# Kernel optimization log

Hardware: AMD Instinct MI355X
Metric: run time of the kernel (lower is better)

The kernel has to match this reference:

```python
import jax, jax.numpy as jnp
import numpy as np

AGENT_TYPE_VEHICLE = 1
AGENT_TYPE_PEDESTRIAN = 2
N_VEHICLE_INTENTIONS = 6
N_PEDESTRIAN_INTENTIONS = 2
INTENTION_LOGIT_DIM = 6


def setup_inputs() -> dict:
    key = jax.random.key(0)
    ks = jax.random.split(key, 10)
    B, N, D = 32, 2048, 512
    H = D // 2
    s_in = 1.0 / np.sqrt(D)
    s_h = 1.0 / np.sqrt(H)
    return {
        "repr3": jax.random.normal(ks[0], (B, N, D), dtype=jnp.float32),
        "agent_type_ids": jax.random.randint(ks[1], (B, N), 0, 4, dtype=jnp.int64),
        # vehicle head: Linear(D, D//2) -> GELU -> Linear(D//2, 6)
        "vW1": jax.random.normal(ks[2], (H, D), dtype=jnp.float32) * s_in,
        "vb1": jax.random.normal(ks[3], (H,), dtype=jnp.float32) * s_in,
        "vW2": jax.random.normal(ks[4], (N_VEHICLE_INTENTIONS, H), dtype=jnp.float32) * s_h,
        "vb2": jax.random.normal(ks[5], (N_VEHICLE_INTENTIONS,), dtype=jnp.float32) * s_h,
        # pedestrian head: Linear(D, D//2) -> GELU -> Linear(D//2, 2)
        "pW1": jax.random.normal(ks[6], (H, D), dtype=jnp.float32) * s_in,
        "pb1": jax.random.normal(ks[7], (H,), dtype=jnp.float32) * s_in,
        "pW2": jax.random.normal(ks[8], (N_PEDESTRIAN_INTENTIONS, H), dtype=jnp.float32) * s_h,
        "pb2": jax.random.normal(ks[9], (N_PEDESTRIAN_INTENTIONS,), dtype=jnp.float32) * s_h,
    }


def _mlp(x, W1, b1, W2, b2):
    # x: [B,N,D] -> [B,N,out]; exact (erf) GELU matches torch nn.GELU()
    h = jax.nn.gelu(jnp.einsum("bnd,hd->bnh", x, W1) + b1, approximate=False)
    return jnp.einsum("bnh,oh->bno", h, W2) + b2


def reference(repr3, agent_type_ids, vW1, vb1, vW2, vb2, pW1, pb1, pW2, pb2):
    v_mask = agent_type_ids == AGENT_TYPE_VEHICLE  # [B,N]
    p_mask = agent_type_ids == AGENT_TYPE_PEDESTRIAN
    v_logits = _mlp(repr3, vW1, vb1, vW2, vb2)  # [B,N,6]
    p_logits = _mlp(repr3, pW1, pb1, pW2, pb2)  # [B,N,2]
    pad = INTENTION_LOGIT_DIM - N_PEDESTRIAN_INTENTIONS
    p_padded = jnp.pad(p_logits, ((0, 0), (0, 0), (0, pad)))  # [B,N,6]
    zero = jnp.zeros((), dtype=repr3.dtype)
    intention_logits = (
        jnp.where(v_mask[..., None], v_logits, zero)
        + jnp.where(p_mask[..., None], p_padded, zero)
    )
    return intention_logits, v_mask, p_mask
```

## Files before the change

### kernel.cpp

```cpp
#include <hip/hip_runtime.h>
#include <hip/hip_bf16.h>
#include <math.h>


#define TOKENS 65536
#define DIM    512
#define HID    256
#define BK     32
#define ASTR   40
#define HSTR   264

using short8 = __attribute__((ext_vector_type(8))) short;
using f32x4  = __attribute__((ext_vector_type(4))) float;

__device__ __forceinline__ unsigned int pkrne(float a, float b) {
    unsigned int ua = __float_as_uint(a);
    unsigned int ub = __float_as_uint(b);
    ua += 0x7FFFu + ((ua >> 16) & 1u);
    ub += 0x7FFFu + ((ub >> 16) & 1u);
    return (ub & 0xFFFF0000u) | (ua >> 16);
}

__device__ __forceinline__ uint2 cvt4(f32x4 v) {
    return make_uint2(pkrne(v[0], v[1]), pkrne(v[2], v[3]));
}

__device__ __forceinline__ short8 cvt8(const float* __restrict__ p) {
    f32x4 a = *(const f32x4*)p;
    f32x4 b = *(const f32x4*)(p + 4);
    union { unsigned int u[4]; short8 s; } r;
    r.u[0] = pkrne(a[0], a[1]);
    r.u[1] = pkrne(a[2], a[3]);
    r.u[2] = pkrne(b[0], b[1]);
    r.u[3] = pkrne(b[2], b[3]);
    return r.s;
}

__device__ __forceinline__ float gelu_exact(float x) {
    return 0.5f * x * (1.0f + erff(x * 0.7071067811865475f));
}

__global__ __launch_bounds__(256, 2)
void intention_heads_kernel(const float* __restrict__ X,
                            const int* __restrict__ ids,
                            const float* __restrict__ vW1,
                            const float* __restrict__ vb1,
                            const float* __restrict__ vW2,
                            const float* __restrict__ vb2,
                            const float* __restrict__ pW1,
                            const float* __restrict__ pb1,
                            const float* __restrict__ pW2,
                            const float* __restrict__ pb2,
                            float* __restrict__ out)
{
    __shared__ __align__(16) unsigned char smem[64 * HSTR * 2];
    __hip_bfloat16* At = (__hip_bfloat16*)smem;
    __hip_bfloat16* Bt = (__hip_bfloat16*)(smem + 64 * ASTR * 2);
    __hip_bfloat16* H  = (__hip_bfloat16*)smem;

    const int bx   = blockIdx.x;
    const int head = bx & 1;
    const int row0 = (bx >> 1) * 64;

    const int tid  = threadIdx.x;
    const int wave = tid >> 6;
    const int lane = tid & 63;
    const int quad = lane >> 4;
    const int l16  = lane & 15;
    const int wcol = wave * 64;

    const float* W1 = head ? pW1 : vW1;
    const float* b1 = head ? pb1 : vb1;

    const int q   = tid & 7;
    const int r0t = tid >> 3;
    const float* Xs  = X  + (long)(row0 + r0t) * DIM + q * 4;
    const float* W1s = W1 + (long)r0t * DIM + q * 4;

    f32x4 pa[2], pb[8];
    #define LOADTILE(k0)                                              \
        do {                                                          \
            pa[0] = *(const f32x4*)(Xs + (k0));                       \
            pa[1] = *(const f32x4*)(Xs + 32 * DIM + (k0));            \
            _Pragma("unroll")                                         \
            for (int e = 0; e < 8; ++e)                               \
                pb[e] = *(const f32x4*)(W1s + e * 32 * DIM + (k0));   \
        } while (0)

    f32x4 acc[4][4];
    #pragma unroll
    for (int i = 0; i < 4; ++i)
        #pragma unroll
        for (int j = 0; j < 4; ++j)
            acc[i][j] = (f32x4){0.f, 0.f, 0.f, 0.f};

    LOADTILE(0);

    for (int it = 0; it < DIM / BK; ++it) {
        *(uint2*)&At[(r0t)      * ASTR + q * 4] = cvt4(pa[0]);
        *(uint2*)&At[(r0t + 32) * ASTR + q * 4] = cvt4(pa[1]);
        #pragma unroll
        for (int e = 0; e < 8; ++e)
            *(uint2*)&Bt[(r0t + 32 * e) * ASTR + q * 4] = cvt4(pb[e]);
        __syncthreads();

        short8 af[4], bf_[4];
        #pragma unroll
        for (int i = 0; i < 4; ++i)
            af[i] = *(const short8*)&At[(i * 16 + l16) * ASTR + quad * 8];
        #pragma unroll
        for (int j = 0; j < 4; ++j)
            bf_[j] = *(const short8*)&Bt[(wcol + j * 16 + l16) * ASTR + quad * 8];

        if (it + 1 < DIM / BK)
            LOADTILE((it + 1) * BK);

        #pragma unroll
        for (int i = 0; i < 4; ++i)
            #pragma unroll
            for (int j = 0; j < 4; ++j)
                acc[i][j] = __builtin_amdgcn_mfma_f32_16x16x32_bf16(af[i], bf_[j], acc[i][j], 0, 0, 0);
        __syncthreads();
    }

    float b1v[4];
    #pragma unroll
    for (int j = 0; j < 4; ++j)
        b1v[j] = b1[wcol + j * 16 + l16];

    #pragma unroll
    for (int i = 0; i < 4; ++i) {
        #pragma unroll
        for (int j = 0; j < 4; ++j) {
            const int col = wcol + j * 16 + l16;
            #pragma unroll
            for (int r = 0; r < 4; ++r) {
                const int row = i * 16 + quad * 4 + r;
                float v = acc[i][j][r] + b1v[j];
                union { unsigned int u; struct { short lo, hi; } s; } t;
                t.u = pkrne(v == v ? gelu_exact(v) : 0.f, 0.f);
                H[row * HSTR + col] = *(__hip_bfloat16*)&t.s.lo;
            }
        }
    }
    __syncthreads();

    const float* W2 = head ? pW2 : vW2;
    const float* b2 = head ? pb2 : vb2;
    const int nOut = head ? 2 : 6;

    f32x4 acc2 = (f32x4){0.f, 0.f, 0.f, 0.f};
    const int tokb = wave * 16;
    const short* hbase = (const short*)&H[(tokb + l16) * HSTR + quad * 8];
    #pragma unroll
    for (int k0 = 0; k0 < HID; k0 += 32) {
        short8 af = *(const short8*)(hbase + k0);
        short8 bfrag = (short8){0, 0, 0, 0, 0, 0, 0, 0};
        if (l16 < nOut)
            bfrag = cvt8(W2 + l16 * HID + k0 + quad * 8);
        acc2 = __builtin_amdgcn_mfma_f32_16x16x32_bf16(af, bfrag, acc2, 0, 0, 0);
    }

    const float b2v = (l16 < nOut) ? b2[l16] : 0.0f;

    #pragma unroll
    for (int r = 0; r < 4; ++r) {
        const int t = row0 + tokb + quad * 4 + r;
        const int type = ids[t];
        if (head == 0) {
            if (l16 == 0) {
                out[TOKENS * 6 + t] = (type == 1) ? 1.0f : 0.0f;
                out[TOKENS * 7 + t] = (type == 2) ? 1.0f : 0.0f;
            }
            if (l16 < 6) {
                if (type == 1)
                    out[t * 6 + l16] = acc2[r] + b2v;
                else if (type != 2)
                    out[t * 6 + l16] = 0.0f;
            }
        } else {
            if (l16 < 6 && type == 2)
                out[t * 6 + l16] = (l16 < 2) ? (acc2[r] + b2v) : 0.0f;
        }
    }
}

extern "C" void kernel_launch(void* const* d_in, const int* in_sizes, int n_in,
                              void* d_out, int out_size, void* d_ws, size_t ws_size,
                              hipStream_t stream) {
    (void)n_in; (void)out_size; (void)d_ws; (void)ws_size;
    const float* X   = (const float*)d_in[0];
    const int*   ids = (const int*)d_in[1];
    const float* vW1 = (const float*)d_in[2];
    const float* vb1 = (const float*)d_in[3];
    const float* vW2 = (const float*)d_in[4];
    const float* vb2 = (const float*)d_in[5];
    const float* pW1 = (const float*)d_in[6];
    const float* pb1 = (const float*)d_in[7];
    const float* pW2 = (const float*)d_in[8];
    const float* pb2 = (const float*)d_in[9];
    float* out = (float*)d_out;

    const int tokens = in_sizes[1];
    const int grid   = (tokens / 64) * 2;

    hipLaunchKernelGGL(intention_heads_kernel, dim3(grid), dim3(256), 0, stream,
                       X, ids, vW1, vb1, vW2, vb2, pW1, pb1, pW2, pb2, out);
}
```

Before: 284.4 us.

## Fuse vehicle and pedestrian heads into one 512-thread block sharing X tile

Each block now computes both heads for its 64 tokens: eight waves cover a combined 512-wide hidden layer made of vW1 and pW1, and X is staged into LDS once instead of once per head. The second-layer waves are split between the vehicle and pedestrian outputs. The register prefetch of the next k-tile is dropped, and launch bounds change to (512,4), which may force register spills given the 64-float accumulators. The LDS footprint grows through the wider H buffer. The bf16 packing now uses a perm builtin, and the NaN guard before GELU is removed.

New measurement: 349.8 us. 1.23x slower.

```diff
diff --git a/kernel.cpp b/kernel.cpp
--- a/kernel.cpp
+++ b/kernel.cpp
@@ -6,9 +6,8 @@
 #define TOKENS 65536
 #define DIM    512
 #define HID    256
-#define BK     32
 #define ASTR   40
-#define HSTR   264
+#define HSTR   520
 
 using short8 = __attribute__((ext_vector_type(8))) short;
 using f32x4  = __attribute__((ext_vector_type(4))) float;
@@ -18,7 +17,7 @@
     unsigned int ub = __float_as_uint(b);
     ua += 0x7FFFu + ((ua >> 16) & 1u);
     ub += 0x7FFFu + ((ub >> 16) & 1u);
-    return (ub & 0xFFFF0000u) | (ua >> 16);
+    return __builtin_amdgcn_perm(ub, ua, 0x07060302u);
 }
 
 __device__ __forceinline__ uint2 cvt4(f32x4 v) {
@@ -28,19 +27,24 @@
 __device__ __forceinline__ short8 cvt8(const float* __restrict__ p) {
     f32x4 a = *(const f32x4*)p;
     f32x4 b = *(const f32x4*)(p + 4);
-    union { unsigned int u[4]; short8 s; } r;
-    r.u[0] = pkrne(a[0], a[1]);
-    r.u[1] = pkrne(a[2], a[3]);
-    r.u[2] = pkrne(b[0], b[1]);
-    r.u[3] = pkrne(b[2], b[3]);
+    union { uint2 u[2]; short8 s; } r;
+    r.u[0] = cvt4(a);
+    r.u[1] = cvt4(b);
     return r.s;
+}
+
+__device__ __forceinline__ __hip_bfloat16 bf16rne(float x) {
+    unsigned int u = __float_as_uint(x);
+    u += 0x7FFFu + ((u >> 16) & 1u);
+    unsigned short hs = (unsigned short)(u >> 16);
+    return *(__hip_bfloat16*)&hs;
 }
 
 __device__ __forceinline__ float gelu_exact(float x) {
     return 0.5f * x * (1.0f + erff(x * 0.7071067811865475f));
 }
 
-__global__ __launch_bounds__(256, 2)
+__global__ __launch_bounds__(512, 4)
 void intention_heads_kernel(const float* __restrict__ X,
                             const int* __restrict__ ids,
                             const float* __restrict__ vW1,
@@ -58,9 +62,7 @@
     __hip_bfloat16* Bt = (__hip_bfloat16*)(smem + 64 * ASTR * 2);
     __hip_bfloat16* H  = (__hip_bfloat16*)smem;
 
-    const int bx   = blockIdx.x;
-    const int head = bx & 1;
-    const int row0 = (bx >> 1) * 64;
+    const int row0 = blockIdx.x * 64;
 
     const int tid  = threadIdx.x;
     const int wave = tid >> 6;
@@ -69,23 +71,11 @@
     const int l16  = lane & 15;
     const int wcol = wave * 64;
 
-    const float* W1 = head ? pW1 : vW1;
-    const float* b1 = head ? pb1 : vb1;
-
-    const int q   = tid & 7;
-    const int r0t = tid >> 3;
-    const float* Xs  = X  + (long)(row0 + r0t) * DIM + q * 4;
-    const float* W1s = W1 + (long)r0t * DIM + q * 4;
-
-    f32x4 pa[2], pb[8];
-    #define LOADTILE(k0)                                              \
-        do {                                                          \
-            pa[0] = *(const f32x4*)(Xs + (k0));                       \
-            pa[1] = *(const f32x4*)(Xs + 32 * DIM + (k0));            \
-            _Pragma("unroll")                                         \
-            for (int e = 0; e < 8; ++e)                               \
-                pb[e] = *(const f32x4*)(W1s + e * 32 * DIM + (k0));   \
-        } while (0)
+    const int q = tid & 7;
+    const int r = tid >> 3;
+    const float* Xs = X   + (long)(row0 + r) * DIM + q * 4;
+    const float* Wv = vW1 + (long)r * DIM + q * 4;
+    const float* Wp = pW1 + (long)r * DIM + q * 4;
 
     f32x4 acc[4][4];
     #pragma unroll
@@ -94,14 +84,21 @@
         for (int j = 0; j < 4; ++j)
             acc[i][j] = (f32x4){0.f, 0.f, 0.f, 0.f};
 
-    LOADTILE(0);
-
-    for (int it = 0; it < DIM / BK; ++it) {
-        *(uint2*)&At[(r0t)      * ASTR + q * 4] = cvt4(pa[0]);
-        *(uint2*)&At[(r0t + 32) * ASTR + q * 4] = cvt4(pa[1]);
-        #pragma unroll
-        for (int e = 0; e < 8; ++e)
-            *(uint2*)&Bt[(r0t + 32 * e) * ASTR + q * 4] = cvt4(pb[e]);
+    for (int k0 = 0; k0 < DIM; k0 += 32) {
+        {
+            f32x4 v = *(const f32x4*)(Xs + k0);
+            *(uint2*)&At[r * ASTR + q * 4] = cvt4(v);
+        }
+        #pragma unroll
+        for (int e = 0; e < 4; ++e) {
+            f32x4 v = *(const f32x4*)(Wv + (long)e * 64 * DIM + k0);
+            *(uint2*)&Bt[(r + 64 * e) * ASTR + q * 4] = cvt4(v);
+        }
+        #pragma unroll
+        for (int e = 0; e < 4; ++e) {
+            f32x4 v = *(const f32x4*)(Wp + (long)e * 64 * DIM + k0);
+            *(uint2*)&Bt[(256 + r + 64 * e) * ASTR + q * 4] = cvt4(v);
+        }
         __syncthreads();
 
         short8 af[4], bf_[4];
@@ -111,9 +108,6 @@
         #pragma unroll
         for (int j = 0; j < 4; ++j)
             bf_[j] = *(const short8*)&Bt[(wcol + j * 16 + l16) * ASTR + quad * 8];
-
-        if (it + 1 < DIM / BK)
-            LOADTILE((it + 1) * BK);
 
         #pragma unroll
         for (int i = 0; i < 4; ++i)
@@ -123,10 +117,12 @@
         __syncthreads();
     }
 
+    const float* b1 = (wave < 4) ? vb1 : pb1;
+    const int    bo = (wave < 4) ? wcol : (wcol - 256);
     float b1v[4];
     #pragma unroll
     for (int j = 0; j < 4; ++j)
-        b1v[j] = b1[wcol + j * 16 + l16];
+        b1v[j] = b1[bo + j * 16 + l16];
 
     #pragma unroll
     for (int i = 0; i < 4; ++i) {
@@ -134,24 +130,24 @@
         for (int j = 0; j < 4; ++j) {
             const int col = wcol + j * 16 + l16;
             #pragma unroll
-            for (int r = 0; r < 4; ++r) {
-                const int row = i * 16 + quad * 4 + r;
-                float v = acc[i][j][r] + b1v[j];
-                union { unsigned int u; struct { short lo, hi; } s; } t;
-                t.u = pkrne(v == v ? gelu_exact(v) : 0.f, 0.f);
-                H[row * HSTR + col] = *(__hip_bfloat16*)&t.s.lo;
+            for (int rr = 0; rr < 4; ++rr) {
+                const int row = i * 16 + quad * 4 + rr;
+                H[row * HSTR + col] = bf16rne(gelu_exact(acc[i][j][rr] + b1v[j]));
             }
         }
     }
     __syncthreads();
 
-    const float* W2 = head ? pW2 : vW2;
-    const float* b2 = head ? pb2 : vb2;
-    const int nOut = head ? 2 : 6;
+    const int g     = wave >> 1;
+    const int isPed = wave & 1;
+    const int tokb  = g * 16;
+    const float* W2 = isPed ? pW2 : vW2;
+    const float* b2 = isPed ? pb2 : vb2;
+    const int  nOut = isPed ? 2 : 6;
+    const int  hoff = isPed ? 256 : 0;
 
     f32x4 acc2 = (f32x4){0.f, 0.f, 0.f, 0.f};
-    const int tokb = wave * 16;
-    const short* hbase = (const short*)&H[(tokb + l16) * HSTR + quad * 8];
+    const short* hbase = (const short*)&H[(tokb + l16) * HSTR + hoff + quad * 8];
     #pragma unroll
     for (int k0 = 0; k0 < HID; k0 += 32) {
         short8 af = *(const short8*)(hbase + k0);
@@ -164,23 +160,23 @@
     const float b2v = (l16 < nOut) ? b2[l16] : 0.0f;
 
     #pragma unroll
-    for (int r = 0; r < 4; ++r) {
-        const int t = row0 + tokb + quad * 4 + r;
+    for (int rr = 0; rr < 4; ++rr) {
+        const int t = row0 + tokb + quad * 4 + rr;
         const int type = ids[t];
-        if (head == 0) {
+        if (!isPed) {
             if (l16 == 0) {
                 out[TOKENS * 6 + t] = (type == 1) ? 1.0f : 0.0f;
                 out[TOKENS * 7 + t] = (type == 2) ? 1.0f : 0.0f;
             }
             if (l16 < 6) {
                 if (type == 1)
-                    out[t * 6 + l16] = acc2[r] + b2v;
+                    out[t * 6 + l16] = acc2[rr] + b2v;
                 else if (type != 2)
                     out[t * 6 + l16] = 0.0f;
             }
         } else {
             if (l16 < 6 && type == 2)
-                out[t * 6 + l16] = (l16 < 2) ? (acc2[r] + b2v) : 0.0f;
+                out[t * 6 + l16] = (l16 < 2) ? (acc2[rr] + b2v) : 0.0f;
         }
     }
 }
@@ -202,8 +198,8 @@
     float* out = (float*)d_out;
 
     const int tokens = in_sizes[1];
-    const int grid   = (tokens / 64) * 2;
-
-    hipLaunchKernelGGL(intention_heads_kernel, dim3(grid), dim3(256), 0, stream,
+    const int grid   = tokens / 64;
+
+    hipLaunchKernelGGL(intention_heads_kernel, dim3(grid), dim3(512), 0, stream,
                        X, ids, vW1, vb1, vW2, vb2, pW1, pb1, pW2, pb2, out);
 }
```
